# Performance work log

Measured on AMD Instinct MI355X. Metric: run time of the kernel, lower is better.

Reference implementation:

```python
import jax, jax.numpy as jnp
import numpy as np


def gcn_conv(x, edge_index, edge_weight, W, b):
    """PyG-style GCNConv: h = x @ W; add self-loops (w=1); sym deg^-1/2 norm;
    scatter-add aggregation; + bias."""
    N = x.shape[0]
    h = x @ W                                   # [N, F_out]
    row, col = edge_index[0], edge_index[1]     # src, dst
    loop = jnp.arange(N)
    row = jnp.concatenate([row, loop])
    col = jnp.concatenate([col, loop])
    ew = jnp.concatenate([edge_weight, jnp.ones((N,), edge_weight.dtype)])
    deg = jax.ops.segment_sum(ew, col, num_segments=N)
    dinv = jnp.where(deg > 0, deg ** -0.5, 0.0)
    norm = dinv[row] * ew * dinv[col]           # [E+N]
    out = jax.ops.segment_sum(h[row] * norm[:, None], col, num_segments=N)
    return out + b


def setup_inputs() -> dict:
    key = jax.random.key(0)
    ks = jax.random.split(key, 12)
    N, F_in, H, O, E = 20000, 3000, 512, 256, 640000
    x = jax.random.normal(ks[0], (N, F_in), dtype=jnp.float32)
    sim_edge_index = jax.random.randint(ks[1], (2, E), 0, N, dtype=jnp.int64)
    sim_edge_weight = jax.random.uniform(ks[2], (E,), dtype=jnp.float32)
    dist_edge_index = jax.random.randint(ks[3], (2, E), 0, N, dtype=jnp.int64)
    dist_edge_weight = jax.random.uniform(ks[4], (E,), dtype=jnp.float32)
    s = 0.02
    return {
        "x": x,
        "sim_edge_index": sim_edge_index,
        "sim_edge_weight": sim_edge_weight,
        "dist_edge_index": dist_edge_index,
        "dist_edge_weight": dist_edge_weight,
        "W1": jax.random.normal(ks[5], (F_in, H), dtype=jnp.float32) * s,
        "b1": jnp.zeros((H,), jnp.float32),
        "W2": jax.random.normal(ks[6], (F_in, H), dtype=jnp.float32) * s,
        "b2": jnp.zeros((H,), jnp.float32),
        "Ws": jax.random.normal(ks[7], (H, O), dtype=jnp.float32) * s,
        "bs": jnp.zeros((O,), jnp.float32),
        "Wd": jax.random.normal(ks[8], (H, O), dtype=jnp.float32) * s,
        "bd": jnp.zeros((O,), jnp.float32),
        "Wf": jax.random.normal(ks[9], (2 * O, O), dtype=jnp.float32) * s,
        "bf": jnp.zeros((O,), jnp.float32),
    }


def reference(x, sim_edge_index, sim_edge_weight, dist_edge_index,
              dist_edge_weight, W1, b1, W2, b2, Ws, bs, Wd, bd, Wf, bf):
    # eval mode: dropout is identity
    xs = jax.nn.relu(gcn_conv(x, sim_edge_index, sim_edge_weight, W1, b1))
    xd = jax.nn.relu(gcn_conv(x, dist_edge_index, dist_edge_weight, W2, b2))
    x_sim = gcn_conv(xs, sim_edge_index, sim_edge_weight, Ws, bs)
    x_dist = gcn_conv(xd, dist_edge_index, dist_edge_weight, Wd, bd)
    fused = jnp.concatenate([x_sim, x_dist], axis=1) @ Wf + bf
    return (x_sim, x_dist, fused)
```

## Files before the change

kernel.cpp:

```cpp
#include <hip/hip_runtime.h>
#include <cstdint>
#include <cstddef>

typedef unsigned short u16;
typedef __bf16 bf16x8 __attribute__((ext_vector_type(8)));
typedef float f32x4 __attribute__((ext_vector_type(4)));

#define N_NODES 20000
#define MPAD    20096
#define E_EDGES 640000
#define K1      3000
#define K1P     3008
#define H_DIM   512
#define NW      1024
#define O_DIM   256

__device__ __forceinline__ float bf2f(unsigned int hi) {
  union { unsigned int u; float f; } v; v.u = hi << 16; return v.f;
}
__device__ __forceinline__ u16 f2bf(float f) {
  union { float f; unsigned int u; } v; v.f = f;
  unsigned int u = v.u;
  return (u16)((u + 0x7fffu + ((u >> 16) & 1u)) >> 16);
}

__device__ __forceinline__ void gl2lds16(const void* g, void* l) {
  __builtin_amdgcn_global_load_lds((const __attribute__((address_space(1))) void*)g,
                                   (__attribute__((address_space(3))) void*)l, 16, 0, 0);
}

__global__ __launch_bounds__(256) void deg_init_k(float* degS, float* degD, int* cntS, int* cntD) {
  int i = blockIdx.x * 256 + threadIdx.x;
  if (i < N_NODES) { degS[i] = 1.0f; degD[i] = 1.0f; cntS[i] = 0; cntD[i] = 0; }
}

__global__ __launch_bounds__(256) void deg_accum_k(const int* eiS, const float* ewS,
                                                   const int* eiD, const float* ewD,
                                                   float* degS, float* degD, int* cntS, int* cntD) {
  int e = blockIdx.x * 256 + threadIdx.x;
  if (e < E_EDGES) {
    int cs = eiS[E_EDGES + e];
    atomicAdd(&degS[cs], ewS[e]);
    atomicAdd(&cntS[cs], 1);
    int cd = eiD[E_EDGES + e];
    atomicAdd(&degD[cd], ewD[e]);
    atomicAdd(&cntD[cd], 1);
  }
}

__global__ __launch_bounds__(256) void dinv_k(const float* degS, const float* degD,
                                              float* dinvS, float* dinvD) {
  int i = blockIdx.x * 256 + threadIdx.x;
  if (i < N_NODES) { dinvS[i] = rsqrtf(degS[i]); dinvD[i] = rsqrtf(degD[i]); }
}

__global__ __launch_bounds__(1024) void scan_k(const int* cntS, int* offS, int* curS,
                                               const int* cntD, int* offD, int* curD) {
  const int* cnt = blockIdx.x ? cntD : cntS;
  int* off = blockIdx.x ? offD : offS;
  int* cur = blockIdx.x ? curD : curS;
  __shared__ int sums[1024];
  const int t = threadIdx.x;
  const int CH = 20;
  int base = t * CH;
  int s = 0;
  for (int j = 0; j < CH; ++j) { int idx = base + j; if (idx < N_NODES) s += cnt[idx]; }
  sums[t] = s;
  __syncthreads();
  for (int d = 1; d < 1024; d <<= 1) {
    int v = (t >= d) ? sums[t - d] : 0;
    __syncthreads();
    sums[t] += v;
    __syncthreads();
  }
  int run = sums[t] - s;
  for (int j = 0; j < CH; ++j) {
    int idx = base + j;
    if (idx <= N_NODES) {
      off[idx] = run; cur[idx] = run;
      if (idx < N_NODES) run += cnt[idx];
    }
  }
}

__global__ __launch_bounds__(256) void scatter_k(const int* eiS, const float* ewS, const float* dinvS,
                                                 int* curS, int* ssrcS, float* snrmS,
                                                 const int* eiD, const float* ewD, const float* dinvD,
                                                 int* curD, int* ssrcD, float* snrmD) {
  int e = blockIdx.x * 256 + threadIdx.x;
  if (e < E_EDGES) {
    {
      int r = eiS[e], c = eiS[E_EDGES + e];
      int pos = atomicAdd(&curS[c], 1);
      ssrcS[pos] = r;
      snrmS[pos] = dinvS[r] * ewS[e] * dinvS[c];
    }
    {
      int r = eiD[e], c = eiD[E_EDGES + e];
      int pos = atomicAdd(&curD[c], 1);
      ssrcD[pos] = r;
      snrmD[pos] = dinvD[r] * ewD[e] * dinvD[c];
    }
  }
}

__global__ __launch_bounds__(256) void conv_x_k(const float* __restrict__ x, u16* __restrict__ xb) {
  const int row = blockIdx.x;
  for (int c = threadIdx.x; c < 376; c += 256) {
    uint4 o = {0, 0, 0, 0};
    if (row < N_NODES && c < 375) {
      const float4* p = (const float4*)(x + (size_t)row * K1 + (size_t)c * 8);
      float4 v0 = p[0], v1 = p[1];
      o.x = f2bf(v0.x) | ((unsigned)f2bf(v0.y) << 16);
      o.y = f2bf(v0.z) | ((unsigned)f2bf(v0.w) << 16);
      o.z = f2bf(v1.x) | ((unsigned)f2bf(v1.y) << 16);
      o.w = f2bf(v1.z) | ((unsigned)f2bf(v1.w) << 16);
    }
    *(uint4*)(xb + (size_t)row * K1P + (size_t)c * 8) = o;
  }
}

__global__ __launch_bounds__(256) void conv_w12_k(const float* __restrict__ W1,
                                                  const float* __restrict__ W2,
                                                  u16* __restrict__ w12t) {
  const int n = blockIdx.x;
  const float* W = (n < H_DIM) ? W1 : W2;
  const int nn = n & (H_DIM - 1);
  for (int k = threadIdx.x; k < K1P; k += 256)
    w12t[(size_t)n * K1P + k] = (k < K1) ? f2bf(W[(size_t)k * H_DIM + nn]) : (u16)0;
}

__global__ __launch_bounds__(256) void conv_wsm_k(const float* Ws, const float* Wd, const float* Wf,
                                                  u16* wst, u16* wdt, u16* wft) {
  const int n = blockIdx.x;
  const int which = blockIdx.y;
  const float* W = (which == 0) ? Ws : (which == 1) ? Wd : Wf;
  u16* o = (which == 0) ? wst : (which == 1) ? wdt : wft;
  for (int k = threadIdx.x; k < H_DIM; k += 256)
    o[(size_t)n * H_DIM + k] = f2bf(W[(size_t)k * O_DIM + n]);
}

template <typename CT, bool BIAS>
__global__ __launch_bounds__(256) void gemm_bt(const u16* __restrict__ A, const u16* __restrict__ Bt,
                                               CT* __restrict__ C, const float* __restrict__ bias,
                                               int Mreal, int K, int ldc) {
  __shared__ alignas(16) u16 As[128 * 64];
  __shared__ alignas(16) u16 Bs[128 * 64];
  const int tid = threadIdx.x;
  const int lane = tid & 63;
  const int wv = tid >> 6;
  const int bm = blockIdx.y * 128;
  const int bn = blockIdx.x * 128;

  const int wm = (wv >> 1) << 6;
  const int wn = (wv & 1) << 6;
  const int frow = lane & 15;
  const int fk = (lane >> 4) << 3;

  const int srow = tid >> 3;
  const int skin = (tid & 7) << 3;
  const u16* ga = A + (size_t)(bm + srow) * K + skin;
  const u16* gb = Bt + (size_t)(bn + srow) * K + skin;
  u16* la = &As[wv * 512];
  u16* lb = &Bs[wv * 512];

  f32x4 acc[4][4] = {};

  for (int k0 = 0; k0 < K; k0 += 64) {
#pragma unroll
    for (int r = 0; r < 4; ++r) {
      gl2lds16(ga + (size_t)(r * 32) * K + k0, la + r * 2048);
      gl2lds16(gb + (size_t)(r * 32) * K + k0, lb + r * 2048);
    }
    __syncthreads();
#pragma unroll
    for (int ks = 0; ks < 64; ks += 32) {
      bf16x8 af[4], bv[4];
#pragma unroll
      for (int t = 0; t < 4; ++t) {
        af[t] = *(const bf16x8*)&As[(wm + t * 16 + frow) * 64 + ks + fk];
        bv[t] = *(const bf16x8*)&Bs[(wn + t * 16 + frow) * 64 + ks + fk];
      }
#pragma unroll
      for (int i = 0; i < 4; ++i)
#pragma unroll
        for (int j = 0; j < 4; ++j)
          acc[i][j] = __builtin_amdgcn_mfma_f32_16x16x32_bf16(af[i], bv[j], acc[i][j], 0, 0, 0);
    }
    __syncthreads();
  }

  const int crow = (lane >> 4) << 2;
  const int ccol = lane & 15;
#pragma unroll
  for (int i = 0; i < 4; ++i) {
#pragma unroll
    for (int r = 0; r < 4; ++r) {
      int gr = bm + wm + i * 16 + crow + r;
      if (gr < Mreal) {
#pragma unroll
        for (int j = 0; j < 4; ++j) {
          int gc = bn + wn + j * 16 + ccol;
          float v = acc[i][j][r];
          if constexpr (BIAS) v += bias[gc];
          if constexpr (sizeof(CT) == 2) C[(size_t)gr * ldc + gc] = (CT)f2bf(v);
          else C[(size_t)gr * ldc + gc] = (CT)v;
        }
      }
    }
  }
}

__global__ __launch_bounds__(256) void agg1_k(const u16* __restrict__ h12,
                                              const int* offS, const int* srcS, const float* nrmS,
                                              const float* dinvS, const float* b1,
                                              const int* offD, const int* srcD, const float* nrmD,
                                              const float* dinvD, const float* b2,
                                              u16* __restrict__ xsd) {
  const int lane = threadIdx.x & 63;
  const int wv = threadIdx.x >> 6;
  const int i = blockIdx.x * 4 + wv;
  const int g = blockIdx.y;
  if (i >= MPAD) return;
  u16* outp = xsd + ((size_t)g * MPAD + i) * H_DIM + lane * 8;
  if (i >= N_NODES) { uint4 z = {0, 0, 0, 0}; *(uint4*)outp = z; return; }

  const int* off = g ? offD : offS;
  const int* src = g ? srcD : srcS;
  const float* nrm = g ? nrmD : nrmS;
  const float* dinv = g ? dinvD : dinvS;
  const float* bias = g ? b2 : b1;
  const size_t cb = (size_t)g * H_DIM + lane * 8;

  float a[8];
  float dv = dinv[i];
  float sw = dv * dv;
  uint4 u = *(const uint4*)(h12 + (size_t)i * NW + cb);
  a[0] = sw * bf2f(u.x & 0xffff); a[1] = sw * bf2f(u.x >> 16);
  a[2] = sw * bf2f(u.y & 0xffff); a[3] = sw * bf2f(u.y >> 16);
  a[4] = sw * bf2f(u.z & 0xffff); a[5] = sw * bf2f(u.z >> 16);
  a[6] = sw * bf2f(u.w & 0xffff); a[7] = sw * bf2f(u.w >> 16);

  const int e0 = off[i], e1 = off[i + 1];
  for (int e = e0; e < e1; ++e) {
    int s = src[e];
    float w = nrm[e];
    uint4 v = *(const uint4*)(h12 + (size_t)s * NW + cb);
    a[0] += w * bf2f(v.x & 0xffff); a[1] += w * bf2f(v.x >> 16);
    a[2] += w * bf2f(v.y & 0xffff); a[3] += w * bf2f(v.y >> 16);
    a[4] += w * bf2f(v.z & 0xffff); a[5] += w * bf2f(v.z >> 16);
    a[6] += w * bf2f(v.w & 0xffff); a[7] += w * bf2f(v.w >> 16);
  }
  float4 bA = *(const float4*)(bias + lane * 8);
  float4 bB = *(const float4*)(bias + lane * 8 + 4);
  a[0] = fmaxf(a[0] + bA.x, 0.f); a[1] = fmaxf(a[1] + bA.y, 0.f);
  a[2] = fmaxf(a[2] + bA.z, 0.f); a[3] = fmaxf(a[3] + bA.w, 0.f);
  a[4] = fmaxf(a[4] + bB.x, 0.f); a[5] = fmaxf(a[5] + bB.y, 0.f);
  a[6] = fmaxf(a[6] + bB.z, 0.f); a[7] = fmaxf(a[7] + bB.w, 0.f);
  uint4 o;
  o.x = f2bf(a[0]) | ((unsigned)f2bf(a[1]) << 16);
  o.y = f2bf(a[2]) | ((unsigned)f2bf(a[3]) << 16);
  o.z = f2bf(a[4]) | ((unsigned)f2bf(a[5]) << 16);
  o.w = f2bf(a[6]) | ((unsigned)f2bf(a[7]) << 16);
  *(uint4*)outp = o;
}

__global__ __launch_bounds__(256) void agg2_k(const u16* __restrict__ hsb, const u16* __restrict__ hdb,
                                              const int* offS, const int* srcS, const float* nrmS,
                                              const float* dinvS, const float* bs,
                                              const int* offD, const int* srcD, const float* nrmD,
                                              const float* dinvD, const float* bd,
                                              float* __restrict__ outF, u16* __restrict__ xcat) {
  const int lane = threadIdx.x & 63;
  const int wv = threadIdx.x >> 6;
  const int i = blockIdx.x * 4 + wv;
  const int g = blockIdx.y;
  if (i >= MPAD) return;
  u16* oc = xcat + (size_t)i * H_DIM + (size_t)g * O_DIM + lane * 4;
  if (i >= N_NODES) { uint2 z = {0, 0}; *(uint2*)oc = z; return; }

  const u16* h = g ? hdb : hsb;
  const int* off = g ? offD : offS;
  const int* src = g ? srcD : srcS;
  const float* nrm = g ? nrmD : nrmS;
  const float* dinv = g ? dinvD : dinvS;
  const float* bias = g ? bd : bs;

  float a[4];
  float dv = dinv[i];
  float sw = dv * dv;
  uint2 u = *(const uint2*)(h + (size_t)i * O_DIM + lane * 4);
  a[0] = sw * bf2f(u.x & 0xffff); a[1] = sw * bf2f(u.x >> 16);
  a[2] = sw * bf2f(u.y & 0xffff); a[3] = sw * bf2f(u.y >> 16);

  const int e0 = off[i], e1 = off[i + 1];
  for (int e = e0; e < e1; ++e) {
    int s = src[e];
    float w = nrm[e];
    uint2 v = *(const uint2*)(h + (size_t)s * O_DIM + lane * 4);
    a[0] += w * bf2f(v.x & 0xffff); a[1] += w * bf2f(v.x >> 16);
    a[2] += w * bf2f(v.y & 0xffff); a[3] += w * bf2f(v.y >> 16);
  }
  float4 bb = *(const float4*)(bias + lane * 4);
  a[0] += bb.x; a[1] += bb.y; a[2] += bb.z; a[3] += bb.w;

  float4 fo = {a[0], a[1], a[2], a[3]};
  *(float4*)(outF + (size_t)g * N_NODES * O_DIM + (size_t)i * O_DIM + lane * 4) = fo;
  uint2 o;
  o.x = f2bf(a[0]) | ((unsigned)f2bf(a[1]) << 16);
  o.y = f2bf(a[2]) | ((unsigned)f2bf(a[3]) << 16);
  *(uint2*)oc = o;
}

extern "C" void kernel_launch(void* const* d_in, const int* in_sizes, int n_in,
                              void* d_out, int out_size, void* d_ws, size_t ws_size,
                              hipStream_t stream) {
  const float* x = (const float*)d_in[0];
  const int* eiS = (const int*)d_in[1];
  const float* ewS = (const float*)d_in[2];
  const int* eiD = (const int*)d_in[3];
  const float* ewD = (const float*)d_in[4];
  const float* W1 = (const float*)d_in[5];
  const float* b1 = (const float*)d_in[6];
  const float* W2 = (const float*)d_in[7];
  const float* b2 = (const float*)d_in[8];
  const float* Ws = (const float*)d_in[9];
  const float* bs = (const float*)d_in[10];
  const float* Wd = (const float*)d_in[11];
  const float* bd = (const float*)d_in[12];
  const float* Wf = (const float*)d_in[13];
  const float* bf_ = (const float*)d_in[14];
  float* out = (float*)d_out;

  char* p = (char*)d_ws;
  auto alloc = [&](size_t n) -> char* { char* r = p; p += (n + 255) & ~(size_t)255; return r; };

  u16* xb    = (u16*)alloc((size_t)MPAD * K1P * 2);
  u16* w12t  = (u16*)alloc((size_t)NW * K1P * 2);
  u16* h12   = (u16*)alloc((size_t)N_NODES * NW * 2);
  u16* xsd   = (u16*)alloc((size_t)2 * MPAD * H_DIM * 2);
  u16* hsb   = (u16*)alloc((size_t)N_NODES * O_DIM * 2);
  u16* hdb   = (u16*)alloc((size_t)N_NODES * O_DIM * 2);
  u16* xcat  = (u16*)alloc((size_t)MPAD * H_DIM * 2);
  u16* wst   = (u16*)alloc((size_t)O_DIM * H_DIM * 2);
  u16* wdt   = (u16*)alloc((size_t)O_DIM * H_DIM * 2);
  u16* wft   = (u16*)alloc((size_t)O_DIM * H_DIM * 2);
  float* degS = (float*)alloc((size_t)N_NODES * 4);
  float* degD = (float*)alloc((size_t)N_NODES * 4);
  float* dinvS = (float*)alloc((size_t)N_NODES * 4);
  float* dinvD = (float*)alloc((size_t)N_NODES * 4);
  int* cntS = (int*)alloc((size_t)N_NODES * 4);
  int* cntD = (int*)alloc((size_t)N_NODES * 4);
  int* offS = (int*)alloc((size_t)(N_NODES + 1) * 4);
  int* offD = (int*)alloc((size_t)(N_NODES + 1) * 4);
  int* curS = (int*)alloc((size_t)(N_NODES + 1) * 4);
  int* curD = (int*)alloc((size_t)(N_NODES + 1) * 4);
  int* ssrcS = (int*)alloc((size_t)E_EDGES * 4);
  int* ssrcD = (int*)alloc((size_t)E_EDGES * 4);
  float* snrmS = (float*)alloc((size_t)E_EDGES * 4);
  float* snrmD = (float*)alloc((size_t)E_EDGES * 4);

  const int gN = (N_NODES + 255) / 256;
  const int gE = (E_EDGES + 255) / 256;

  deg_init_k<<<gN, 256, 0, stream>>>(degS, degD, cntS, cntD);
  deg_accum_k<<<gE, 256, 0, stream>>>(eiS, ewS, eiD, ewD, degS, degD, cntS, cntD);
  dinv_k<<<gN, 256, 0, stream>>>(degS, degD, dinvS, dinvD);
  scan_k<<<2, 1024, 0, stream>>>(cntS, offS, curS, cntD, offD, curD);
  scatter_k<<<gE, 256, 0, stream>>>(eiS, ewS, dinvS, curS, ssrcS, snrmS,
                                    eiD, ewD, dinvD, curD, ssrcD, snrmD);

  conv_x_k<<<MPAD, 256, 0, stream>>>(x, xb);
  conv_w12_k<<<NW, 256, 0, stream>>>(W1, W2, w12t);
  conv_wsm_k<<<dim3(O_DIM, 3), 256, 0, stream>>>(Ws, Wd, Wf, wst, wdt, wft);

  gemm_bt<u16, false><<<dim3(8, 157), 256, 0, stream>>>(xb, w12t, h12, nullptr, N_NODES, K1P, NW);

  agg1_k<<<dim3(MPAD / 4, 2), 256, 0, stream>>>(h12, offS, ssrcS, snrmS, dinvS, b1,
                                                offD, ssrcD, snrmD, dinvD, b2, xsd);

  gemm_bt<u16, false><<<dim3(2, 157), 256, 0, stream>>>(xsd, wst, hsb, nullptr, N_NODES, H_DIM, O_DIM);
  gemm_bt<u16, false><<<dim3(2, 157), 256, 0, stream>>>(xsd + (size_t)MPAD * H_DIM, wdt, hdb, nullptr,
                                                        N_NODES, H_DIM, O_DIM);

  agg2_k<<<dim3(MPAD / 4, 2), 256, 0, stream>>>(hsb, hdb, offS, ssrcS, snrmS, dinvS, bs,
                                                offD, ssrcD, snrmD, dinvD, bd, out, xcat);

  gemm_bt<float, true><<<dim3(2, 157), 256, 0, stream>>>(xcat, wft, out + (size_t)2 * N_NODES * O_DIM,
                                                         bf_, N_NODES, H_DIM, O_DIM);
}
```

Measured before the change: 1.229 ms.

## Tile weight transposes through shared memory and XOR-swizzle GEMM LDS layout

Replaces the per-column strided weight transpose kernels with 64x64 shared-memory tiled transposes, so both the global reads and the writes are coalesced. It also applies an XOR swizzle to the GEMM's LDS tile layout, on both the global-to-LDS store side and the fragment read side, to avoid bank conflicts on the bf16x8 fragment loads. The swizzle must agree exactly between writer and reader; otherwise the GEMM results would be wrong. The padded K region of the weights is still zero-filled by the tile bounds check.

```diff
diff --git a/kernel.cpp b/kernel.cpp
--- a/kernel.cpp
+++ b/kernel.cpp
@@ -123,21 +123,50 @@
 __global__ __launch_bounds__(256) void conv_w12_k(const float* __restrict__ W1,
                                                   const float* __restrict__ W2,
                                                   u16* __restrict__ w12t) {
-  const int n = blockIdx.x;
-  const float* W = (n < H_DIM) ? W1 : W2;
-  const int nn = n & (H_DIM - 1);
-  for (int k = threadIdx.x; k < K1P; k += 256)
-    w12t[(size_t)n * K1P + k] = (k < K1) ? f2bf(W[(size_t)k * H_DIM + nn]) : (u16)0;
+  __shared__ float t[64][65];
+  const int kb = blockIdx.x;
+  const int nb = blockIdx.y;
+  const int n0 = nb * 64;
+  const float* W = (n0 < H_DIM) ? W1 : W2;
+  const int nn0 = n0 & (H_DIM - 1);
+  const int k0 = kb * 64;
+  const int tc = threadIdx.x & 63;
+  const int tr4 = threadIdx.x >> 6;
+#pragma unroll
+  for (int rr = 0; rr < 16; ++rr) {
+    int r = tr4 * 16 + rr;
+    int k = k0 + r;
+    t[r][tc] = (k < K1) ? W[(size_t)k * H_DIM + nn0 + tc] : 0.f;
+  }
+  __syncthreads();
+#pragma unroll
+  for (int rr = 0; rr < 16; ++rr) {
+    int n = tr4 * 16 + rr;
+    w12t[(size_t)(n0 + n) * K1P + k0 + tc] = f2bf(t[tc][n]);
+  }
 }
 
 __global__ __launch_bounds__(256) void conv_wsm_k(const float* Ws, const float* Wd, const float* Wf,
                                                   u16* wst, u16* wdt, u16* wft) {
-  const int n = blockIdx.x;
-  const int which = blockIdx.y;
+  __shared__ float t[64][65];
+  const int which = blockIdx.z;
   const float* W = (which == 0) ? Ws : (which == 1) ? Wd : Wf;
   u16* o = (which == 0) ? wst : (which == 1) ? wdt : wft;
-  for (int k = threadIdx.x; k < H_DIM; k += 256)
-    o[(size_t)n * H_DIM + k] = f2bf(W[(size_t)k * O_DIM + n]);
+  const int k0 = blockIdx.x * 64;
+  const int n0 = blockIdx.y * 64;
+  const int tc = threadIdx.x & 63;
+  const int tr4 = threadIdx.x >> 6;
+#pragma unroll
+  for (int rr = 0; rr < 16; ++rr) {
+    int r = tr4 * 16 + rr;
+    t[r][tc] = W[(size_t)(k0 + r) * O_DIM + n0 + tc];
+  }
+  __syncthreads();
+#pragma unroll
+  for (int rr = 0; rr < 16; ++rr) {
+    int n = tr4 * 16 + rr;
+    o[(size_t)(n0 + n) * H_DIM + k0 + tc] = f2bf(t[tc][n]);
+  }
 }
 
 template <typename CT, bool BIAS>
@@ -155,12 +184,13 @@
   const int wm = (wv >> 1) << 6;
   const int wn = (wv & 1) << 6;
   const int frow = lane & 15;
-  const int fk = (lane >> 4) << 3;
+  const int q = lane >> 4;
+  const int r7 = lane & 7;
 
   const int srow = tid >> 3;
-  const int skin = (tid & 7) << 3;
-  const u16* ga = A + (size_t)(bm + srow) * K + skin;
-  const u16* gb = Bt + (size_t)(bn + srow) * K + skin;
+  const int sgr = ((tid & 7) ^ ((tid >> 3) & 7)) << 3;
+  const u16* ga = A + (size_t)(bm + srow) * K + sgr;
+  const u16* gb = Bt + (size_t)(bn + srow) * K + sgr;
   u16* la = &As[wv * 512];
   u16* lb = &Bs[wv * 512];
 
@@ -175,11 +205,12 @@
     __syncthreads();
 #pragma unroll
     for (int ks = 0; ks < 64; ks += 32) {
+      const int p = (((q + (ks >> 3)) ^ r7) << 3);
       bf16x8 af[4], bv[4];
 #pragma unroll
       for (int t = 0; t < 4; ++t) {
-        af[t] = *(const bf16x8*)&As[(wm + t * 16 + frow) * 64 + ks + fk];
-        bv[t] = *(const bf16x8*)&Bs[(wn + t * 16 + frow) * 64 + ks + fk];
+        af[t] = *(const bf16x8*)&As[(wm + t * 16 + frow) * 64 + p];
+        bv[t] = *(const bf16x8*)&Bs[(wn + t * 16 + frow) * 64 + p];
       }
 #pragma unroll
       for (int i = 0; i < 4; ++i)
@@ -371,8 +402,8 @@
                                     eiD, ewD, dinvD, curD, ssrcD, snrmD);
 
   conv_x_k<<<MPAD, 256, 0, stream>>>(x, xb);
-  conv_w12_k<<<NW, 256, 0, stream>>>(W1, W2, w12t);
-  conv_wsm_k<<<dim3(O_DIM, 3), 256, 0, stream>>>(Ws, Wd, Wf, wst, wdt, wft);
+  conv_w12_k<<<dim3(47, 16), 256, 0, stream>>>(W1, W2, w12t);
+  conv_wsm_k<<<dim3(8, 4, 3), 256, 0, stream>>>(Ws, Wd, Wf, wst, wdt, wft);
 
   gemm_bt<u16, false><<<dim3(8, 157), 256, 0, stream>>>(xb, w12t, h12, nullptr, N_NODES, K1P, NW);
 
```

New measurement: 1.134 ms. 1.08x faster.
